# Kernel optimization log

Hardware: AMD Instinct MI355X
Metric: run time of the kernel (lower is better)

Reference implementation:

```python
import jax, jax.numpy as jnp
import numpy as np

B, S, H = 2, 2048, 1024
NH, HD = 16, 64
WINDOW = 512
NEG = -10000.0


def setup_inputs() -> dict:
    key = jax.random.key(0)
    ks = jax.random.split(key, 8)
    sc = 0.02
    return {
        "hidden_states": jax.random.normal(ks[0], (B, S, H), dtype=jnp.float32),
        "attention_mask": jnp.zeros((B, 1, 1, S), dtype=jnp.float32),
        "Wq": jax.random.normal(ks[1], (H, H), dtype=jnp.float32) * sc,
        "bq": jnp.zeros((H,), dtype=jnp.float32),
        "Wk": jax.random.normal(ks[2], (H, H), dtype=jnp.float32) * sc,
        "bk": jnp.zeros((H,), dtype=jnp.float32),
        "Wv": jax.random.normal(ks[3], (H, H), dtype=jnp.float32) * sc,
        "bv": jnp.zeros((H,), dtype=jnp.float32),
    }


def _heads(x):
    # [b, t, (h d)] -> [b, h, t, d]
    b, t, _ = x.shape
    return x.reshape(b, t, NH, HD).transpose(0, 2, 1, 3)


def reference(hidden_states, attention_mask, Wq, bq, Wk, bk, Wv, bv):
    q = _heads(hidden_states @ Wq.T + bq)
    k = _heads(hidden_states @ Wk.T + bk)
    v = _heads(hidden_states @ Wv.T + bv)

    # Faithful mask construction (note: window mask is triu(diag=-WINDOW),
    # penalizing the recent window, exactly as in the source).
    i = jnp.arange(S)[:, None]
    j = jnp.arange(S)[None, :]
    causal_mask = jnp.where(j > i, NEG, 0.0).astype(jnp.float32)          # triu, diag=1
    window_mask = jnp.where(j >= i - WINDOW, NEG, 0.0).astype(jnp.float32)  # triu, diag=-512
    mask = causal_mask + window_mask + attention_mask  # [b,1,S,S]

    scale = 1.0 / jnp.sqrt(jnp.asarray(HD, dtype=q.dtype))
    scores = jnp.einsum("bhtd,bhsd->bhts", q, k) * scale + mask  # [b,h,S,S]
    probs = jax.nn.softmax(scores, axis=-1)
    out = jnp.einsum("bhts,bhsd->bhtd", probs, v)  # [b,h,S,d]
    # [b,h,t,d] -> [b,t,(h d)]
    return out.transpose(0, 2, 1, 3).reshape(B, S, H)
```

## Files before the change

kernel.cpp:

```cpp
#include <hip/hip_runtime.h>

typedef float f32x2 __attribute__((ext_vector_type(2)));
typedef float f32x4 __attribute__((ext_vector_type(4)));
typedef float f32x16 __attribute__((ext_vector_type(16)));
typedef _Float16 half8 __attribute__((ext_vector_type(8)));
typedef _Float16 half4 __attribute__((ext_vector_type(4)));
typedef unsigned int u32;
typedef u32 u32x4 __attribute__((ext_vector_type(4)));

#define S_LEN 2048
#define NHEAD 16
#define HDIM 64
#define BATCH 2
#define WINDOW 512
#define M2_FIX 5.770780163555852f
#define LOG2E 1.4426950408889634f

#define GLDS16(gp, lp) __builtin_amdgcn_global_load_lds( \
    (const __attribute__((address_space(1))) void*)(gp), \
    (__attribute__((address_space(3))) void*)(lp), 16, 0, 0)


__global__ __launch_bounds__(256) void convert_kernel(
    const float4* __restrict__ hs, const float4* __restrict__ wq,
    const float4* __restrict__ wk, const float4* __restrict__ wv,
    _Float16* __restrict__ hsb, _Float16* __restrict__ wb) {
  int i = blockIdx.x * 256 + threadIdx.x;
  float4 v;
  _Float16* dst;
  if (i < 1048576) {
    v = hs[i];
    dst = hsb + (size_t)i * 4;
  } else {
    int j = i - 1048576;
    if (j < 262144) v = wq[j];
    else if (j < 524288) v = wk[j - 262144];
    else v = wv[j - 524288];
    dst = wb + (size_t)j * 4;
  }
  half4 o;
  o[0] = (_Float16)v.x; o[1] = (_Float16)v.y;
  o[2] = (_Float16)v.z; o[3] = (_Float16)v.w;
  *(half4*)dst = o;
}

__global__ __launch_bounds__(256) void qkv_gemm(
    const _Float16* __restrict__ A, const _Float16* __restrict__ W,
    const float* __restrict__ bq, const float* __restrict__ bk,
    const float* __restrict__ bv,
    _Float16* __restrict__ Qf, _Float16* __restrict__ Kf, _Float16* __restrict__ Vf) {
  __shared__ _Float16 sbuf[2][16384];
  const int tid = threadIdx.x;
  const int wv = tid >> 6;
  const int lane = tid & 63;
  const int g = lane >> 4;
  const int c = lane & 15;
  const int b = blockIdx.x;
  const int slot = b >> 3;
  const int n0 = ((b & 7) * 3 + (slot >> 5)) * 128;
  const int m0 = (slot & 31) * 128;
  const int wm = (wv & 1) * 64;
  const int wn = (wv >> 1) * 64;

  const int srow8 = lane >> 3;
  const int sslot = lane & 7;
  const int lsl = sslot ^ srow8;
  const int rA = wv * 32 + srow8;
  const _Float16* aS = A + (size_t)(m0 + rA) * 1024 + lsl * 8;
  const _Float16* bS = W + (size_t)(n0 + rA) * 1024 + lsl * 8;

  const int rcolA0 = wv * 32 * 64;

  f32x4 acc[4][4];
#pragma unroll
  for (int i = 0; i < 4; ++i)
#pragma unroll
    for (int j = 0; j < 4; ++j) acc[i][j] = (f32x4){0.f, 0.f, 0.f, 0.f};

  auto STAGE = [&](int bf_, int k0) __attribute__((always_inline)) {
    char* aD = (char*)&sbuf[bf_][rcolA0];
    char* bD = (char*)&sbuf[bf_][8192 + rcolA0];
#pragma unroll
    for (int grp = 0; grp < 4; ++grp) {
      GLDS16(aS + grp * 8192 + k0, aD + grp * 1024);
      GLDS16(bS + grp * 8192 + k0, bD + grp * 1024);
    }
  };

  STAGE(0, 0);
  __syncthreads();
  int cur = 0;

  for (int t = 0; t < 16; ++t) {
    if (t < 15) STAGE(cur ^ 1, (t + 1) * 64);
    const _Float16* Asb = &sbuf[cur][0];
    const _Float16* Bsb = &sbuf[cur][8192];
    half8 af[4][2];
#pragma unroll
    for (int mf = 0; mf < 4; ++mf) {
      const int row = wm + mf * 16 + c;
#pragma unroll
      for (int ch = 0; ch < 2; ++ch)
        af[mf][ch] = *(const half8*)&Asb[row * 64 + ((ch * 4 + g) ^ (c & 7)) * 8];
    }
#pragma unroll
    for (int nf = 0; nf < 4; ++nf) {
      const int row = wn + nf * 16 + c;
      half8 bf0 = *(const half8*)&Bsb[row * 64 + ((g) ^ (c & 7)) * 8];
      half8 bf1 = *(const half8*)&Bsb[row * 64 + ((4 + g) ^ (c & 7)) * 8];
#pragma unroll
      for (int mf = 0; mf < 4; ++mf) {
        acc[mf][nf] = __builtin_amdgcn_mfma_f32_16x16x32_f16(af[mf][0], bf0, acc[mf][nf], 0, 0, 0);
        acc[mf][nf] = __builtin_amdgcn_mfma_f32_16x16x32_f16(af[mf][1], bf1, acc[mf][nf], 0, 0, 0);
      }
    }
    __syncthreads();
    cur ^= 1;
  }

  const int kind = n0 >> 10;
  const int nb = (n0 + wn) & 1023;
  const int head = nb >> 6;
  const float* bias = kind == 0 ? bq : (kind == 1 ? bk : bv);
  _Float16* dst = kind == 0 ? Qf : (kind == 1 ? Kf : Vf);
  _Float16* ob = &sbuf[0][wv * 4096];

  if (kind < 2) {
    const float scl = kind == 0 ? (0.125f * LOG2E) : 1.0f;
#pragma unroll
    for (int nf = 0; nf < 4; ++nf) {
      const int d = nf * 16 + c;
      const float bsv = bias[nb + d];
      const int base = nf * 512 + ((c >> 3) & 1) * 256 + (c & 7);
#pragma unroll
      for (int mf = 0; mf < 4; ++mf) {
#pragma unroll
        for (int r = 0; r < 4; ++r) {
          ob[(mf >> 1) * 2048 + base + (mf & 1) * 128 + g * 32 + r * 8] =
              (_Float16)((acc[mf][nf][r] + bsv) * scl);
        }
      }
    }
  } else {
#pragma unroll
    for (int nf = 0; nf < 4; ++nf) {
      const int d = nf * 16 + c;
      const float bsv = bias[nb + d];
#pragma unroll
      for (int mf = 0; mf < 4; ++mf) {
        half4 v4;
#pragma unroll
        for (int r = 0; r < 4; ++r) v4[r] = (_Float16)(acc[mf][nf][r] + bsv);
        *(half4*)&ob[(mf >> 1) * 2048 + ((nf >> 1) * 2 + (mf & 1)) * 512 +
                     ((g >> 1) * 32 + (nf & 1) * 16 + c) * 8 + (g & 1) * 4] = v4;
      }
    }
  }

  const int bI = (m0 + wm) >> 11;
  const size_t gbase = (size_t)(bI * NHEAD + head) * 131072 +
                       (size_t)(((m0 + wm) & 2047) >> 5) * 2048;
#pragma unroll
  for (int i = 0; i < 8; ++i) {
    half8 v = *(const half8*)&ob[i * 512 + lane * 8];
    *(half8*)&dst[gbase + i * 512 + lane * 8] = v;
  }
}

__global__ __launch_bounds__(256) void attn_kernel(
    const _Float16* __restrict__ Qf, const _Float16* __restrict__ Kf,
    const _Float16* __restrict__ Vf, const float* __restrict__ amask,
    float* __restrict__ out) {
  __shared__ _Float16 obuf[4][32][72];
  __shared__ float lbuf[4][32];
  const int tid = threadIdx.x;
  const int w = tid >> 6;
  const int lane = tid & 63;
  const int q31 = lane & 31;
  const int h = lane >> 5;
  const int bid = blockIdx.x;
  const int bh = bid & 31;
  const int idx = 63 - (bid >> 5);
  const int i0 = idx * 32;
  const int bI = bh >> 4;
  const int head = bh & 15;

  const _Float16* Qh = Qf + (size_t)bh * 131072;
  const _Float16* Kh = Kf + (size_t)bh * 131072;
  const _Float16* Vh = Vf + (size_t)bh * 131072;
  const float* am = amask + (size_t)bI * S_LEN;

  const int q = i0 + q31;
  const int hiq = (q <= WINDOW) ? q : (q - WINDOW - 1);
  const int last = i0 + 31;
  const int himax = (last <= WINDOW) ? last
                    : ((i0 <= WINDOW) ? WINDOW : (last - WINDOW - 1));
  const int hiq_min = (last <= WINDOW) ? i0
                      : ((i0 > WINDOW) ? (i0 - WINDOW - 1) : 0);
  const int ntiles = (himax >> 5) + 1;
  const int nfull = (hiq_min + 1) >> 5;
  const int lim = hiq - 4 * h;

  half8 qf[4];
#pragma unroll
  for (int ch = 0; ch < 4; ++ch)
    qf[ch] = *(const half8*)&Qh[(size_t)idx * 2048 + ch * 512 + lane * 8];

  f32x16 zero16, m2init;
#pragma unroll
  for (int r = 0; r < 16; ++r) { zero16[r] = 0.f; m2init[r] = -M2_FIX; }
  f32x16 oacc0 = zero16, oacc1 = zero16;
  f32x2 lp[4];
#pragma unroll
  for (int r = 0; r < 4; ++r) lp[r] = (f32x2){0.f, 0.f};

  auto computeTile = [&](half8 k0, half8 k1, half8 k2, half8 k3, int t)
      __attribute__((always_inline)) {
    const int j0 = t * 32;
    const _Float16* vt = Vh + (size_t)t * 2048 + lane * 8;
    half8 vf0 = *(const half8*)&vt[0];
    half8 vf1 = *(const half8*)&vt[512];
    half8 vf2 = *(const half8*)&vt[1024];
    half8 vf3 = *(const half8*)&vt[1536];
    f32x4 amv[4];
#pragma unroll
    for (int s4 = 0; s4 < 4; ++s4)
      amv[s4] = *(const f32x4*)&am[j0 + 8 * s4 + 4 * h];

    __builtin_amdgcn_s_setprio(1);
    f32x16 st = __builtin_amdgcn_mfma_f32_32x32x16_f16(k0, qf[0], m2init, 0, 0, 0);
    st = __builtin_amdgcn_mfma_f32_32x32x16_f16(k1, qf[1], st, 0, 0, 0);
    st = __builtin_amdgcn_mfma_f32_32x32x16_f16(k2, qf[2], st, 0, 0, 0);
    st = __builtin_amdgcn_mfma_f32_32x32x16_f16(k3, qf[3], st, 0, 0, 0);
    __builtin_amdgcn_s_setprio(0);

    float p[16];
#pragma unroll
    for (int r = 0; r < 16; ++r)
      p[r] = __builtin_fmaf(amv[r >> 2][r & 3], LOG2E, st[r]);
    if (t >= nfull) {
      const int lm = lim - j0;
#pragma unroll
      for (int r = 0; r < 16; ++r) {
        const int off = (r & 3) + 8 * (r >> 2);
        p[r] = (off <= lm) ? p[r] : -3e38f;
      }
    }
#pragma unroll
    for (int r = 0; r < 16; ++r) p[r] = __builtin_amdgcn_exp2f(p[r]);
#pragma unroll
    for (int j = 0; j < 4; ++j) {
      lp[j] += (f32x2){p[2 * j], p[2 * j + 1]};
      lp[j] += (f32x2){p[8 + 2 * j], p[9 + 2 * j]};
    }

    u32 pk[8];
#pragma unroll
    for (int r = 0; r < 8; ++r) {
      auto c2 = __builtin_amdgcn_cvt_pkrtz(p[2 * r], p[2 * r + 1]);
      pk[r] = __builtin_bit_cast(u32, c2);
    }
    u32 a0 = pk[0], b0 = pk[2];
    u32 a1 = pk[1], b1 = pk[3];
    u32 a2 = pk[4], b2 = pk[6];
    u32 a3 = pk[5], b3 = pk[7];
    asm("v_permlane32_swap_b32 %0, %1" : "+v"(a0), "+v"(b0));
    asm("v_permlane32_swap_b32 %0, %1" : "+v"(a1), "+v"(b1));
    asm("v_permlane32_swap_b32 %0, %1" : "+v"(a2), "+v"(b2));
    asm("v_permlane32_swap_b32 %0, %1" : "+v"(a3), "+v"(b3));
    const half8 pf0 = __builtin_bit_cast(half8, (u32x4){a0, a1, b0, b1});
    const half8 pf1 = __builtin_bit_cast(half8, (u32x4){a2, a3, b2, b3});

    __builtin_amdgcn_s_setprio(1);
    oacc0 = __builtin_amdgcn_mfma_f32_32x32x16_f16(vf0, pf0, oacc0, 0, 0, 0);
    oacc0 = __builtin_amdgcn_mfma_f32_32x32x16_f16(vf1, pf1, oacc0, 0, 0, 0);
    oacc1 = __builtin_amdgcn_mfma_f32_32x32x16_f16(vf2, pf0, oacc1, 0, 0, 0);
    oacc1 = __builtin_amdgcn_mfma_f32_32x32x16_f16(vf3, pf1, oacc1, 0, 0, 0);
    __builtin_amdgcn_s_setprio(0);
  };

#define LOADK(d0, d1, d2, d3, tt)                                        \
  {                                                                      \
    const _Float16* kt = Kh + (size_t)(tt) * 2048 + lane * 8;            \
    d0 = *(const half8*)&kt[0];                                          \
    d1 = *(const half8*)&kt[512];                                        \
    d2 = *(const half8*)&kt[1024];                                       \
    d3 = *(const half8*)&kt[1536];                                       \
  }

  int t = w;
  if (t < ntiles) {
    half8 k0, k1, k2, k3;
    LOADK(k0, k1, k2, k3, t);
    int tn = t + 4;
    while (tn < ntiles) {
      half8 n0, n1, n2, n3;
      LOADK(n0, n1, n2, n3, tn);
      computeTile(k0, k1, k2, k3, t);
      k0 = n0; k1 = n1; k2 = n2; k3 = n3;
      t = tn;
      tn += 4;
    }
    computeTile(k0, k1, k2, k3, t);
  }

  f32x2 s2 = (lp[0] + lp[1]) + (lp[2] + lp[3]);
  float lw = s2[0] + s2[1];
  lw += __shfl_xor(lw, 32);
  if (h == 0) lbuf[w][q31] = lw;
#pragma unroll
  for (int j = 0; j < 4; ++j) {
    half4 h0, h1;
#pragma unroll
    for (int e = 0; e < 4; ++e) {
      h0[e] = (_Float16)oacc0[4 * j + e];
      h1[e] = (_Float16)oacc1[4 * j + e];
    }
    *(half4*)&obuf[w][q31][4 * h + 8 * j]      = h0;
    *(half4*)&obuf[w][q31][32 + 4 * h + 8 * j] = h1;
  }
  __syncthreads();

  const int mq = tid >> 3;
  const int md = (tid & 7) * 8;
  const float lt = (lbuf[0][mq] + lbuf[1][mq]) + (lbuf[2][mq] + lbuf[3][mq]);
  float s[8];
  half8 p0 = *(const half8*)&obuf[0][mq][md];
#pragma unroll
  for (int e = 0; e < 8; ++e) s[e] = (float)p0[e];
#pragma unroll
  for (int w4 = 1; w4 < 4; ++w4) {
    half8 pw = *(const half8*)&obuf[w4][mq][md];
#pragma unroll
    for (int e = 0; e < 8; ++e) s[e] += (float)pw[e];
  }
  const float inv = 1.0f / lt;
  float4 s0, s1;
  s0.x = s[0] * inv; s0.y = s[1] * inv; s0.z = s[2] * inv; s0.w = s[3] * inv;
  s1.x = s[4] * inv; s1.y = s[5] * inv; s1.z = s[6] * inv; s1.w = s[7] * inv;
  float* op = out + ((size_t)(bI * S_LEN + i0 + mq)) * 1024 + head * 64 + md;
  *(float4*)op = s0;
  *(float4*)(op + 4) = s1;
}

extern "C" void kernel_launch(void* const* d_in, const int* in_sizes, int n_in,
                              void* d_out, int out_size, void* d_ws, size_t ws_size,
                              hipStream_t stream) {
  const float* hs = (const float*)d_in[0];
  const float* am = (const float*)d_in[1];
  const float* Wq = (const float*)d_in[2];
  const float* bq = (const float*)d_in[3];
  const float* Wk = (const float*)d_in[4];
  const float* bk = (const float*)d_in[5];
  const float* Wv = (const float*)d_in[6];
  const float* bv = (const float*)d_in[7];
  float* out = (float*)d_out;

  char* ws = (char*)d_ws;
  _Float16* hsb = (_Float16*)(ws);
  _Float16* wb  = (_Float16*)(ws + 8388608);
  _Float16* Qf  = (_Float16*)(ws + 14680064);
  _Float16* Kf  = (_Float16*)(ws + 23068672);
  _Float16* Vf  = (_Float16*)(ws + 31457280);

  convert_kernel<<<7168, 256, 0, stream>>>(
      (const float4*)hs, (const float4*)Wq, (const float4*)Wk, (const float4*)Wv, hsb, wb);
  qkv_gemm<<<768, 256, 0, stream>>>(hsb, wb, bq, bk, bv, Qf, Kf, Vf);
  attn_kernel<<<2048, 256, 0, stream>>>(Qf, Kf, Vf, am, out);
}
```

Measured before the change: 77.10 us.

## Remap block indices for XCD L2 locality and prefetch V tiles with K

The QKV GEMM block-to-tile mapping is changed so each XCD handles a contiguous group of M rows and N columns, which is meant to improve L2 reuse of A and W tiles. The attention kernel's head mapping is also remapped so blocks for the same (batch, head) land on the same XCD. V tiles are now prefetched one iteration ahead together with K rather than loaded inside the compute step. The prefetch raises register pressure and could reduce occupancy.

```diff
diff --git a/kernel.cpp b/kernel.cpp
--- a/kernel.cpp
+++ b/kernel.cpp
@@ -56,9 +56,12 @@
   const int g = lane >> 4;
   const int c = lane & 15;
   const int b = blockIdx.x;
-  const int slot = b >> 3;
-  const int n0 = ((b & 7) * 3 + (slot >> 5)) * 128;
-  const int m0 = (slot & 31) * 128;
+  const int xcd = b & 7;
+  const int s = b >> 3;
+  const int sub = s / 48;
+  const int rem = s - sub * 48;
+  const int m0 = (((xcd >> 1) << 3) + rem / 6) * 128;
+  const int n0 = ((xcd & 1) * 12 + sub * 6 + rem % 6) * 128;
   const int wm = (wv & 1) * 64;
   const int wn = (wv >> 1) * 64;
 
@@ -179,7 +182,8 @@
   const int q31 = lane & 31;
   const int h = lane >> 5;
   const int bid = blockIdx.x;
-  const int bh = bid & 31;
+  const int xcd = bid & 7;
+  const int bh = xcd * 4 + ((bid >> 3) & 3);
   const int idx = 63 - (bid >> 5);
   const int i0 = idx * 32;
   const int bI = bh >> 4;
@@ -214,14 +218,10 @@
 #pragma unroll
   for (int r = 0; r < 4; ++r) lp[r] = (f32x2){0.f, 0.f};
 
-  auto computeTile = [&](half8 k0, half8 k1, half8 k2, half8 k3, int t)
+  auto computeTile = [&](half8 k0, half8 k1, half8 k2, half8 k3,
+                         half8 vf0, half8 vf1, half8 vf2, half8 vf3, int t)
       __attribute__((always_inline)) {
     const int j0 = t * 32;
-    const _Float16* vt = Vh + (size_t)t * 2048 + lane * 8;
-    half8 vf0 = *(const half8*)&vt[0];
-    half8 vf1 = *(const half8*)&vt[512];
-    half8 vf2 = *(const half8*)&vt[1024];
-    half8 vf3 = *(const half8*)&vt[1536];
     f32x4 amv[4];
 #pragma unroll
     for (int s4 = 0; s4 < 4; ++s4)
@@ -279,29 +279,35 @@
     __builtin_amdgcn_s_setprio(0);
   };
 
-#define LOADK(d0, d1, d2, d3, tt)                                        \
+#define LOADKV(k0, k1, k2, k3, v0, v1, v2, v3, tt)                       \
   {                                                                      \
     const _Float16* kt = Kh + (size_t)(tt) * 2048 + lane * 8;            \
-    d0 = *(const half8*)&kt[0];                                          \
-    d1 = *(const half8*)&kt[512];                                        \
-    d2 = *(const half8*)&kt[1024];                                       \
-    d3 = *(const half8*)&kt[1536];                                       \
+    const _Float16* vt = Vh + (size_t)(tt) * 2048 + lane * 8;            \
+    k0 = *(const half8*)&kt[0];                                          \
+    k1 = *(const half8*)&kt[512];                                        \
+    k2 = *(const half8*)&kt[1024];                                       \
+    k3 = *(const half8*)&kt[1536];                                       \
+    v0 = *(const half8*)&vt[0];                                          \
+    v1 = *(const half8*)&vt[512];                                        \
+    v2 = *(const half8*)&vt[1024];                                       \
+    v3 = *(const half8*)&vt[1536];                                       \
   }
 
   int t = w;
   if (t < ntiles) {
-    half8 k0, k1, k2, k3;
-    LOADK(k0, k1, k2, k3, t);
+    half8 k0, k1, k2, k3, v0, v1, v2, v3;
+    LOADKV(k0, k1, k2, k3, v0, v1, v2, v3, t);
     int tn = t + 4;
     while (tn < ntiles) {
-      half8 n0, n1, n2, n3;
-      LOADK(n0, n1, n2, n3, tn);
-      computeTile(k0, k1, k2, k3, t);
+      half8 n0, n1, n2, n3, u0, u1, u2, u3;
+      LOADKV(n0, n1, n2, n3, u0, u1, u2, u3, tn);
+      computeTile(k0, k1, k2, k3, v0, v1, v2, v3, t);
       k0 = n0; k1 = n1; k2 = n2; k3 = n3;
+      v0 = u0; v1 = u1; v2 = u2; v3 = u3;
       t = tn;
       tn += 4;
     }
-    computeTile(k0, k1, k2, k3, t);
+    computeTile(k0, k1, k2, k3, v0, v1, v2, v3, t);
   }
 
   f32x2 s2 = (lp[0] + lp[1]) + (lp[2] + lp[3]);
```

New measurement: 77.17 us. No clear change (+0.1%).

## Process two query strips per attention block and remap GEMM tiles per XCD

Applied to the files above, without the earlier changes.

Each attention workgroup now handles two adjacent 32-row query strips, so every K/V tile and mask chunk it loads serves both strips. The grid is halved to 1024 blocks. The QKV GEMM block-to-tile mapping is also changed so blocks on the same XCD cover a compact M×N region, which should improve L2 reuse. The costs are more registers from doubled accumulators, fewer blocks in flight, and extra syncthreads in the epilogue.

```diff
diff --git a/kernel.cpp b/kernel.cpp
--- a/kernel.cpp
+++ b/kernel.cpp
@@ -56,9 +56,12 @@
   const int g = lane >> 4;
   const int c = lane & 15;
   const int b = blockIdx.x;
-  const int slot = b >> 3;
-  const int n0 = ((b & 7) * 3 + (slot >> 5)) * 128;
-  const int m0 = (slot & 31) * 128;
+  const int xcd = b & 7;
+  const int s = b >> 3;
+  const int sub = s / 48;
+  const int rem = s - sub * 48;
+  const int m0 = (((xcd >> 1) << 3) + rem / 6) * 128;
+  const int n0 = ((xcd & 1) * 12 + sub * 6 + rem % 6) * 128;
   const int wm = (wv & 1) * 64;
   const int wn = (wv >> 1) * 64;
 
@@ -68,7 +71,6 @@
   const int rA = wv * 32 + srow8;
   const _Float16* aS = A + (size_t)(m0 + rA) * 1024 + lsl * 8;
   const _Float16* bS = W + (size_t)(n0 + rA) * 1024 + lsl * 8;
-
   const int rcolA0 = wv * 32 * 64;
 
   f32x4 acc[4][4];
@@ -180,8 +182,9 @@
   const int h = lane >> 5;
   const int bid = blockIdx.x;
   const int bh = bid & 31;
-  const int idx = 63 - (bid >> 5);
-  const int i0 = idx * 32;
+  const int pp = bid >> 5;
+  const int idxA = 63 - 2 * pp;
+  const int idxB = 62 - 2 * pp;
   const int bI = bh >> 4;
   const int head = bh & 15;
 
@@ -190,43 +193,44 @@
   const _Float16* Vh = Vf + (size_t)bh * 131072;
   const float* am = amask + (size_t)bI * S_LEN;
 
-  const int q = i0 + q31;
-  const int hiq = (q <= WINDOW) ? q : (q - WINDOW - 1);
-  const int last = i0 + 31;
-  const int himax = (last <= WINDOW) ? last
-                    : ((i0 <= WINDOW) ? WINDOW : (last - WINDOW - 1));
-  const int hiq_min = (last <= WINDOW) ? i0
-                      : ((i0 > WINDOW) ? (i0 - WINDOW - 1) : 0);
-  const int ntiles = (himax >> 5) + 1;
-  const int nfull = (hiq_min + 1) >> 5;
-  const int lim = hiq - 4 * h;
-
-  half8 qf[4];
-#pragma unroll
-  for (int ch = 0; ch < 4; ++ch)
-    qf[ch] = *(const half8*)&Qh[(size_t)idx * 2048 + ch * 512 + lane * 8];
-
-  f32x16 zero16, m2init;
-#pragma unroll
-  for (int r = 0; r < 16; ++r) { zero16[r] = 0.f; m2init[r] = -M2_FIX; }
-  f32x16 oacc0 = zero16, oacc1 = zero16;
-  f32x2 lp[4];
-#pragma unroll
-  for (int r = 0; r < 4; ++r) lp[r] = (f32x2){0.f, 0.f};
-
-  auto computeTile = [&](half8 k0, half8 k1, half8 k2, half8 k3, int t)
+  auto stripParams = [&](int idx, int& nt, int& nfull, int& lim)
       __attribute__((always_inline)) {
+    const int i0 = idx * 32;
+    const int q = i0 + q31;
+    const int hiq = (q <= WINDOW) ? q : (q - WINDOW - 1);
+    const int last = i0 + 31;
+    const int himax = (last <= WINDOW) ? last
+                      : ((i0 <= WINDOW) ? WINDOW : (last - WINDOW - 1));
+    const int hiq_min = (last <= WINDOW) ? i0
+                        : ((i0 > WINDOW) ? (i0 - WINDOW - 1) : 0);
+    nt = (himax >> 5) + 1;
+    nfull = (hiq_min + 1) >> 5;
+    lim = hiq - 4 * h;
+  };
+  int ntA, nfullA, limA, ntB, nfullB, limB;
+  stripParams(idxA, ntA, nfullA, limA);
+  stripParams(idxB, ntB, nfullB, limB);
+  const int tmax = ntA > ntB ? ntA : ntB;
+
+  half8 qfA[4], qfB[4];
+#pragma unroll
+  for (int ch = 0; ch < 4; ++ch) {
+    qfA[ch] = *(const half8*)&Qh[(size_t)idxA * 2048 + ch * 512 + lane * 8];
+    qfB[ch] = *(const half8*)&Qh[(size_t)idxB * 2048 + ch * 512 + lane * 8];
+  }
+
+  f32x16 m2init;
+#pragma unroll
+  for (int r = 0; r < 16; ++r) m2init[r] = -M2_FIX;
+  f32x16 oA0 = {}, oA1 = {}, oB0 = {}, oB1 = {};
+  f32x2 lpA[4] = {}, lpB[4] = {};
+
+  auto doStrip = [&](f32x16& o0, f32x16& o1, f32x2* lp, const half8* qf,
+                     int lim, int nfull, int t,
+                     half8 k0, half8 k1, half8 k2, half8 k3,
+                     half8 v0, half8 v1, half8 v2, half8 v3,
+                     const f32x4* amv) __attribute__((always_inline)) {
     const int j0 = t * 32;
-    const _Float16* vt = Vh + (size_t)t * 2048 + lane * 8;
-    half8 vf0 = *(const half8*)&vt[0];
-    half8 vf1 = *(const half8*)&vt[512];
-    half8 vf2 = *(const half8*)&vt[1024];
-    half8 vf3 = *(const half8*)&vt[1536];
-    f32x4 amv[4];
-#pragma unroll
-    for (int s4 = 0; s4 < 4; ++s4)
-      amv[s4] = *(const f32x4*)&am[j0 + 8 * s4 + 4 * h];
-
     __builtin_amdgcn_s_setprio(1);
     f32x16 st = __builtin_amdgcn_mfma_f32_32x32x16_f16(k0, qf[0], m2init, 0, 0, 0);
     st = __builtin_amdgcn_mfma_f32_32x32x16_f16(k1, qf[1], st, 0, 0, 0);
@@ -272,14 +276,14 @@
     const half8 pf1 = __builtin_bit_cast(half8, (u32x4){a2, a3, b2, b3});
 
     __builtin_amdgcn_s_setprio(1);
-    oacc0 = __builtin_amdgcn_mfma_f32_32x32x16_f16(vf0, pf0, oacc0, 0, 0, 0);
-    oacc0 = __builtin_amdgcn_mfma_f32_32x32x16_f16(vf1, pf1, oacc0, 0, 0, 0);
-    oacc1 = __builtin_amdgcn_mfma_f32_32x32x16_f16(vf2, pf0, oacc1, 0, 0, 0);
-    oacc1 = __builtin_amdgcn_mfma_f32_32x32x16_f16(vf3, pf1, oacc1, 0, 0, 0);
+    o0 = __builtin_amdgcn_mfma_f32_32x32x16_f16(v0, pf0, o0, 0, 0, 0);
+    o0 = __builtin_amdgcn_mfma_f32_32x32x16_f16(v1, pf1, o0, 0, 0, 0);
+    o1 = __builtin_amdgcn_mfma_f32_32x32x16_f16(v2, pf0, o1, 0, 0, 0);
+    o1 = __builtin_amdgcn_mfma_f32_32x32x16_f16(v3, pf1, o1, 0, 0, 0);
     __builtin_amdgcn_s_setprio(0);
   };
 
-#define LOADK(d0, d1, d2, d3, tt)                                        \
+#define LOADK4(d0, d1, d2, d3, tt)                                       \
   {                                                                      \
     const _Float16* kt = Kh + (size_t)(tt) * 2048 + lane * 8;            \
     d0 = *(const half8*)&kt[0];                                          \
@@ -289,58 +293,77 @@
   }
 
   int t = w;
-  if (t < ntiles) {
+  if (t < tmax) {
     half8 k0, k1, k2, k3;
-    LOADK(k0, k1, k2, k3, t);
-    int tn = t + 4;
-    while (tn < ntiles) {
+    LOADK4(k0, k1, k2, k3, t);
+    for (;;) {
+      const int tn = t + 4;
+      const bool more = tn < tmax;
       half8 n0, n1, n2, n3;
-      LOADK(n0, n1, n2, n3, tn);
-      computeTile(k0, k1, k2, k3, t);
+      if (more) LOADK4(n0, n1, n2, n3, tn);
+      const _Float16* vt = Vh + (size_t)t * 2048 + lane * 8;
+      half8 v0 = *(const half8*)&vt[0];
+      half8 v1 = *(const half8*)&vt[512];
+      half8 v2 = *(const half8*)&vt[1024];
+      half8 v3 = *(const half8*)&vt[1536];
+      f32x4 amv[4];
+#pragma unroll
+      for (int s4 = 0; s4 < 4; ++s4)
+        amv[s4] = *(const f32x4*)&am[t * 32 + 8 * s4 + 4 * h];
+
+      if (t < ntA)
+        doStrip(oA0, oA1, lpA, qfA, limA, nfullA, t, k0, k1, k2, k3, v0, v1, v2, v3, amv);
+      if (t < ntB)
+        doStrip(oB0, oB1, lpB, qfB, limB, nfullB, t, k0, k1, k2, k3, v0, v1, v2, v3, amv);
+
+      if (!more) break;
       k0 = n0; k1 = n1; k2 = n2; k3 = n3;
       t = tn;
-      tn += 4;
-    }
-    computeTile(k0, k1, k2, k3, t);
-  }
-
-  f32x2 s2 = (lp[0] + lp[1]) + (lp[2] + lp[3]);
-  float lw = s2[0] + s2[1];
-  lw += __shfl_xor(lw, 32);
-  if (h == 0) lbuf[w][q31] = lw;
-#pragma unroll
-  for (int j = 0; j < 4; ++j) {
-    half4 h0, h1;
-#pragma unroll
-    for (int e = 0; e < 4; ++e) {
-      h0[e] = (_Float16)oacc0[4 * j + e];
-      h1[e] = (_Float16)oacc1[4 * j + e];
-    }
-    *(half4*)&obuf[w][q31][4 * h + 8 * j]      = h0;
-    *(half4*)&obuf[w][q31][32 + 4 * h + 8 * j] = h1;
-  }
-  __syncthreads();
-
-  const int mq = tid >> 3;
-  const int md = (tid & 7) * 8;
-  const float lt = (lbuf[0][mq] + lbuf[1][mq]) + (lbuf[2][mq] + lbuf[3][mq]);
-  float s[8];
-  half8 p0 = *(const half8*)&obuf[0][mq][md];
-#pragma unroll
-  for (int e = 0; e < 8; ++e) s[e] = (float)p0[e];
-#pragma unroll
-  for (int w4 = 1; w4 < 4; ++w4) {
-    half8 pw = *(const half8*)&obuf[w4][mq][md];
-#pragma unroll
-    for (int e = 0; e < 8; ++e) s[e] += (float)pw[e];
-  }
-  const float inv = 1.0f / lt;
-  float4 s0, s1;
-  s0.x = s[0] * inv; s0.y = s[1] * inv; s0.z = s[2] * inv; s0.w = s[3] * inv;
-  s1.x = s[4] * inv; s1.y = s[5] * inv; s1.z = s[6] * inv; s1.w = s[7] * inv;
-  float* op = out + ((size_t)(bI * S_LEN + i0 + mq)) * 1024 + head * 64 + md;
-  *(float4*)op = s0;
-  *(float4*)(op + 4) = s1;
+    }
+  }
+
+  auto finish = [&](f32x16& o0, f32x16& o1, f32x2* lp, int idx)
+      __attribute__((always_inline)) {
+    f32x2 s2 = (lp[0] + lp[1]) + (lp[2] + lp[3]);
+    float lw = s2[0] + s2[1];
+    lw += __shfl_xor(lw, 32);
+    if (h == 0) lbuf[w][q31] = lw;
+#pragma unroll
+    for (int j = 0; j < 4; ++j) {
+      half4 h0, h1;
+#pragma unroll
+      for (int e = 0; e < 4; ++e) {
+        h0[e] = (_Float16)o0[4 * j + e];
+        h1[e] = (_Float16)o1[4 * j + e];
+      }
+      *(half4*)&obuf[w][q31][4 * h + 8 * j]      = h0;
+      *(half4*)&obuf[w][q31][32 + 4 * h + 8 * j] = h1;
+    }
+    __syncthreads();
+    const int mq = tid >> 3;
+    const int md = (tid & 7) * 8;
+    const float lt = (lbuf[0][mq] + lbuf[1][mq]) + (lbuf[2][mq] + lbuf[3][mq]);
+    float s[8];
+    half8 p0 = *(const half8*)&obuf[0][mq][md];
+#pragma unroll
+    for (int e = 0; e < 8; ++e) s[e] = (float)p0[e];
+#pragma unroll
+    for (int w4 = 1; w4 < 4; ++w4) {
+      half8 pw = *(const half8*)&obuf[w4][mq][md];
+#pragma unroll
+      for (int e = 0; e < 8; ++e) s[e] += (float)pw[e];
+    }
+    const float inv = 1.0f / lt;
+    float4 s0, s1;
+    s0.x = s[0] * inv; s0.y = s[1] * inv; s0.z = s[2] * inv; s0.w = s[3] * inv;
+    s1.x = s[4] * inv; s1.y = s[5] * inv; s1.z = s[6] * inv; s1.w = s[7] * inv;
+    float* op = out + ((size_t)(bI * S_LEN + idx * 32 + mq)) * 1024 + head * 64 + md;
+    *(float4*)op = s0;
+    *(float4*)(op + 4) = s1;
+    __syncthreads();
+  };
+  finish(oA0, oA1, lpA, idxA);
+  finish(oB0, oB1, lpB, idxB);
 }
 
 extern "C" void kernel_launch(void* const* d_in, const int* in_sizes, int n_in,
@@ -366,5 +389,5 @@
   convert_kernel<<<7168, 256, 0, stream>>>(
       (const float4*)hs, (const float4*)Wq, (const float4*)Wk, (const float4*)Wv, hsb, wb);
   qkv_gemm<<<768, 256, 0, stream>>>(hsb, wb, bq, bk, bv, Qf, Kf, Vf);
-  attn_kernel<<<2048, 256, 0, stream>>>(Qf, Kf, Vf, am, out);
+  attn_kernel<<<1024, 256, 0, stream>>>(Qf, Kf, Vf, am, out);
 }
```

Result: slower. 86.72 us (+12.5%).
